# Performance work log

Measured on AMD Instinct MI355X. Metric: run time of the kernel, lower is better.

Reference implementation:

```python
import jax, jax.numpy as jnp
import numpy as np

N_LAYERS, H, D, DFF, V = 6, 16, 1024, 4096, 512
B, S = 4, 2048
DK = D // H
EPS = 1e-6
NEG = -1000000000.0


def _pe_table(max_len, d):
    pos = np.arange(max_len, dtype=np.float32)[:, None]
    div = 1.0 / (10000.0 ** (np.arange(0, d, 2, dtype=np.float32) / d))
    pe = np.zeros((max_len, d), dtype=np.float32)
    pe[:, 0::2] = np.sin(pos * div)
    pe[:, 1::2] = np.cos(pos * div)
    return jnp.asarray(pe[None])  # [1, max_len, d]


def setup_inputs() -> dict:
    key = jax.random.key(0)
    ks = jax.random.split(key, 20)
    f = lambda k, shp: (jax.random.normal(k, shp, dtype=jnp.float32) * 0.02)
    inp = {
        "tgt": jax.random.randint(ks[0], (B, S), 0, V, dtype=jnp.int64),
        "tgt_mask": jnp.tril(jnp.ones((S, S), dtype=jnp.int32))[None],  # [1,S,S] causal
        "emb": f(ks[1], (V, D)),
        "pe": _pe_table(S, D),
        "Wq": f(ks[2], (N_LAYERS, H, D, DK)), "bq": f(ks[3], (N_LAYERS, H, DK)),
        "Wk": f(ks[4], (N_LAYERS, H, D, DK)), "bk": f(ks[5], (N_LAYERS, H, DK)),
        "Wv": f(ks[6], (N_LAYERS, H, D, DK)), "bv": f(ks[7], (N_LAYERS, H, DK)),
        "Wo": f(ks[8], (N_LAYERS, D, D)), "bo": f(ks[9], (N_LAYERS, D)),
        "W1": f(ks[10], (N_LAYERS, D, DFF)), "b1": f(ks[11], (N_LAYERS, DFF)),
        "W2": f(ks[12], (N_LAYERS, DFF, D)), "b2": f(ks[13], (N_LAYERS, D)),
        "ln1_a": jnp.ones((N_LAYERS, D)), "ln1_b": jnp.zeros((N_LAYERS, D)),
        "ln2_a": jnp.ones((N_LAYERS, D)), "ln2_b": jnp.zeros((N_LAYERS, D)),
        "lnf_a": jnp.ones((D,)), "lnf_b": jnp.zeros((D,)),
    }
    return inp


def _ln(x, a, b):
    # torch: a*(x-mean)/(std+eps)+b with unbiased std
    m = x.mean(-1, keepdims=True)
    var = ((x - m) ** 2).sum(-1, keepdims=True) / (x.shape[-1] - 1)
    return a * (x - m) / (jnp.sqrt(var) + EPS) + b


def reference(tgt, tgt_mask, emb, pe, Wq, bq, Wk, bk, Wv, bv, Wo, bo,
              W1, b1, W2, b2, ln1_a, ln1_b, ln2_a, ln2_b, lnf_a, lnf_b):
    d = emb.shape[1]
    s = tgt.shape[1]
    x = emb[tgt] * jnp.sqrt(jnp.float32(d)) + pe[:, :s]  # [B,S,D]
    dk = Wq.shape[-1]
    scale = jnp.sqrt(jnp.float32(dk))

    def layer(x, p):
        wq, bq_, wk, bk_, wv, bv_, wo, bo_, w1, b1_, w2, b2_, a1, g1, a2, g2 = p
        h = _ln(x, a1, g1)
        q = jnp.einsum('bsd,hdk->bhsk', h, wq) + bq_[:, None, :]
        k = jnp.einsum('bsd,hdk->bhsk', h, wk) + bk_[:, None, :]
        v = jnp.einsum('bsd,hdk->bhsk', h, wv) + bv_[:, None, :]
        sc = jnp.einsum('bhsk,bhtk->bhst', q, k) / scale
        sc = jnp.where(tgt_mask[:, None] == 0, jnp.float32(NEG), sc)
        att = jax.nn.softmax(sc, axis=-1)
        o = jnp.einsum('bhst,bhtk->bhsk', att, v)
        o = o.transpose(0, 2, 1, 3).reshape(x.shape)  # concat heads (head order)
        x = x + (o @ wo + bo_)
        h2 = _ln(x, a2, g2)
        x = x + (jnp.maximum(h2 @ w1 + b1_, 0.0) @ w2 + b2_)
        return x, None

    x, _ = jax.lax.scan(layer, x, (Wq, bq, Wk, bk, Wv, bv, Wo, bo,
                                   W1, b1, W2, b2, ln1_a, ln1_b, ln2_a, ln2_b))
    return _ln(x, lnf_a, lnf_b)
```

## Files before the change

kernel.cpp:

```cpp
#include <hip/hip_runtime.h>

typedef __bf16 bf16;
typedef float f32x4 __attribute__((ext_vector_type(4)));
typedef __bf16 bf16x8 __attribute__((ext_vector_type(8)));
typedef __bf16 bf16x4 __attribute__((ext_vector_type(4)));
typedef __bf16 bf16x2 __attribute__((ext_vector_type(2)));

#define NL 6
#define NH 16
#define DM 1024
#define DFF 4096
#define SEQ 2048
#define NB 4
#define NTOK (NB*SEQ)

__device__ __forceinline__ void gload16(const void* g, void* l) {
  __builtin_amdgcn_global_load_lds((const __attribute__((address_space(1))) void*)g,
                                   (__attribute__((address_space(3))) void*)l, 16, 0, 0);
}

__global__ __launch_bounds__(256) void repack_t(const float* __restrict__ src,
                                                bf16* __restrict__ out, int K, int N) {
  const int l = blockIdx.z;
  const int d0 = blockIdx.x * 32, n0 = blockIdx.y * 32;
  __shared__ float t[32][33];
  const int tx = threadIdx.x & 31, ty = threadIdx.x >> 5;
  const float* s = src + (size_t)l * K * N;
  #pragma unroll
  for (int j = 0; j < 4; ++j)
    t[ty*4 + j][tx] = s[(size_t)(d0 + ty*4 + j) * N + n0 + tx];
  __syncthreads();
  bf16* o = out + (size_t)l * N * K;
  #pragma unroll
  for (int j = 0; j < 4; ++j)
    o[(size_t)(n0 + ty*4 + j) * K + d0 + tx] = (bf16)t[tx][ty*4 + j];
}

__global__ __launch_bounds__(256) void repack_qkv(const float* __restrict__ Wq,
                                                  const float* __restrict__ Wk,
                                                  const float* __restrict__ Wv,
                                                  bf16* __restrict__ out) {
  const int l = blockIdx.z;
  const int d0 = blockIdx.x * 32, n0 = blockIdx.y * 32;
  __shared__ float t[32][33];
  const int tx = threadIdx.x & 31, ty = threadIdx.x >> 5;
  const int which = n0 >> 10, h = (n0 & 1023) >> 6, kh0 = n0 & 63;
  const float* W = (which == 0) ? Wq : (which == 1 ? Wk : Wv);
  const float* s = W + ((size_t)(l*NH + h) * DM) * 64 + kh0;
  #pragma unroll
  for (int j = 0; j < 4; ++j)
    t[ty*4 + j][tx] = s[(size_t)(d0 + ty*4 + j) * 64 + tx];
  __syncthreads();
  bf16* o = out + (size_t)l * 3072 * DM + (size_t)n0 * DM + d0;
  #pragma unroll
  for (int j = 0; j < 4; ++j)
    o[(size_t)(ty*4 + j) * DM + tx] = (bf16)t[tx][ty*4 + j];
}

__global__ __launch_bounds__(256) void repack_b(const float* __restrict__ bq,
                                                const float* __restrict__ bk,
                                                const float* __restrict__ bv,
                                                float* __restrict__ out) {
  const int i = blockIdx.x * 256 + threadIdx.x;
  if (i >= NL * 3072) return;
  const int l = i / 3072, n = i % 3072;
  const int which = n >> 10, h = (n >> 6) & 15, kh = n & 63;
  const float* b = (which == 0) ? bq : (which == 1 ? bk : bv);
  out[i] = b[(l*NH + h) * 64 + kh];
}

__global__ __launch_bounds__(256) void embed_k(const int* __restrict__ tgt,
                                               const float* __restrict__ emb,
                                               const float* __restrict__ pe,
                                               float* __restrict__ x) {
  const int i = blockIdx.x;
  const int spos = i & (SEQ - 1);
  const int tok = tgt[i];
  const int tid = threadIdx.x;
  float4 e = ((const float4*)(emb + (size_t)tok * DM))[tid];
  float4 p = ((const float4*)(pe + (size_t)spos * DM))[tid];
  float4 r; r.x = e.x*32.f + p.x; r.y = e.y*32.f + p.y; r.z = e.z*32.f + p.z; r.w = e.w*32.f + p.w;
  ((float4*)(x + (size_t)i * DM))[tid] = r;
}

template<bool OB>
__global__ __launch_bounds__(256) void ln_k(const float* __restrict__ x,
                                            const float* __restrict__ a,
                                            const float* __restrict__ bsh,
                                            bf16* __restrict__ ob, float* __restrict__ of) {
  __shared__ float red[8];
  const int row = blockIdx.x, tid = threadIdx.x;
  const float4 v = ((const float4*)(x + (size_t)row * DM))[tid];
  float s = v.x + v.y + v.z + v.w;
  #pragma unroll
  for (int off = 32; off > 0; off >>= 1) s += __shfl_down(s, off);
  if ((tid & 63) == 0) red[tid >> 6] = s;
  __syncthreads();
  const float mean = (red[0] + red[1] + red[2] + red[3]) * (1.f / 1024.f);
  const float d0 = v.x - mean, d1 = v.y - mean, d2 = v.z - mean, d3 = v.w - mean;
  float ss = d0*d0 + d1*d1 + d2*d2 + d3*d3;
  #pragma unroll
  for (int off = 32; off > 0; off >>= 1) ss += __shfl_down(ss, off);
  if ((tid & 63) == 0) red[4 + (tid >> 6)] = ss;
  __syncthreads();
  const float var = (red[4] + red[5] + red[6] + red[7]) * (1.f / 1023.f);
  const float inv = 1.f / (sqrtf(var) + 1e-6f);
  const float4 av = ((const float4*)a)[tid];
  const float4 bv = ((const float4*)bsh)[tid];
  const float r0 = av.x * d0 * inv + bv.x;
  const float r1 = av.y * d1 * inv + bv.y;
  const float r2 = av.z * d2 * inv + bv.z;
  const float r3 = av.w * d3 * inv + bv.w;
  if (OB) {
    bf16x4 w; w[0] = (bf16)r0; w[1] = (bf16)r1; w[2] = (bf16)r2; w[3] = (bf16)r3;
    ((bf16x4*)(ob + (size_t)row * DM))[tid] = w;
  } else {
    float4 w; w.x = r0; w.y = r1; w.z = r2; w.w = r3;
    ((float4*)(of + (size_t)row * DM))[tid] = w;
  }
}

#define BARRIER() asm volatile("s_barrier" ::: "memory")
#define VMW(n)    asm volatile("s_waitcnt vmcnt(" #n ")" ::: "memory")

template<int EPI>
__global__ __launch_bounds__(512, 1) void gemm8(const bf16* __restrict__ A,
                                                const bf16* __restrict__ B,
                                                const float* __restrict__ bias,
                                                float* __restrict__ xres,
                                                bf16* __restrict__ outb,
                                                bf16* __restrict__ vtb,
                                                int K, int ldc) {
  __shared__ __align__(16) char lds[131072];
  const int tid = threadIdx.x;
  const int m0 = blockIdx.x * 256, n0 = blockIdx.y * 256;
  const int wid = tid >> 6, lane = tid & 63;
  const int wm = wid >> 2, wn = wid & 3;
  const int fr = lane & 15, fq = lane >> 4;
  const int fl16 = (fq * 16 + fr) * 16;
  const int s0 = tid, s1 = tid + 512;
  const int r0 = ((s0 >> 7) << 4) | (s0 & 15), c0 = (((s0 >> 6) & 1) << 2) | ((s0 >> 4) & 3);
  const int r1 = ((s1 >> 7) << 4) | (s1 & 15), c1 = (((s1 >> 6) & 1) << 2) | ((s1 >> 4) & 3);
  const bf16* Ap0 = A + (size_t)(m0 + r0) * K + c0 * 8;
  const bf16* Ap1 = A + (size_t)(m0 + r1) * K + c1 * 8;
  const bf16* Bp0 = B + (size_t)(n0 + r0) * K + c0 * 8;
  const bf16* Bp1 = B + (size_t)(n0 + r1) * K + c1 * 8;
  const size_t rskip = (size_t)128 * K;
  const int aRd = wm * 16384;
  const int bRd = 32768 + (wn >> 1) * 16384;
  const int bN = (wn & 1) * 4;

  f32x4 acc[8][4] = {};
  bf16x8 af8[8][2], bfr[4][2];

#define ST_A(d, h, kt) { \
  gload16(Ap0 + (size_t)(h) * rskip + (kt), lds + (d)*65536 + (h)*16384 + s0*16); \
  gload16(Ap1 + (size_t)(h) * rskip + (kt), lds + (d)*65536 + (h)*16384 + s1*16); }
#define ST_B(d, h, kt) { \
  gload16(Bp0 + (size_t)(h) * rskip + (kt), lds + (d)*65536 + 32768 + (h)*16384 + s0*16); \
  gload16(Bp1 + (size_t)(h) * rskip + (kt), lds + (d)*65536 + 32768 + (h)*16384 + s1*16); }
#define LD_A(d, mb) { _Pragma("unroll") for (int m_ = 0; m_ < 4; ++m_) \
    _Pragma("unroll") for (int ks_ = 0; ks_ < 2; ++ks_) \
      af8[(mb) + m_][ks_] = *(const bf16x8*)(lds + (d)*65536 + aRd + ((mb) + m_)*2048 + ks_*1024 + fl16); }
#define LD_B(d, nb) { _Pragma("unroll") for (int n_ = 0; n_ < 2; ++n_) \
    _Pragma("unroll") for (int ks_ = 0; ks_ < 2; ++ks_) \
      bfr[(nb) + n_][ks_] = *(const bf16x8*)(lds + (d)*65536 + bRd + (bN + (nb) + n_)*2048 + ks_*1024 + fl16); }
#define MFMA_Q(mb, nb) { __builtin_amdgcn_s_setprio(1); \
  _Pragma("unroll") for (int m_ = 0; m_ < 4; ++m_) \
  _Pragma("unroll") for (int n_ = 0; n_ < 2; ++n_) \
  _Pragma("unroll") for (int ks_ = 0; ks_ < 2; ++ks_) \
    acc[(mb) + m_][(nb) + n_] = __builtin_amdgcn_mfma_f32_16x16x32_bf16( \
        af8[(mb) + m_][ks_], bfr[(nb) + n_][ks_], acc[(mb) + m_][(nb) + n_], 0, 0, 0); \
  __builtin_amdgcn_s_setprio(0); }

  ST_A(0, 0, 0); ST_A(0, 1, 0);
  ST_B(0, 0, 0); ST_B(0, 1, 0);
  ST_A(1, 0, 64); ST_A(1, 1, 64);
  VMW(4);
  BARRIER();

  const int niter = K >> 7;
  for (int it = 0; it < niter; ++it) {
    const int ktB1 = (2 * it + 1) << 6;
    const int ktE2 = (2 * it + 2) << 6;
    const int ktO3 = (2 * it + 3) << 6;
    const bool more = (it + 1 < niter);
    LD_A(0, 0); LD_B(0, 0);
    ST_B(1, 0, ktB1);
    BARRIER(); MFMA_Q(0, 0); BARRIER();
    LD_A(0, 4);
    ST_B(1, 1, ktB1);
    BARRIER(); MFMA_Q(4, 0); BARRIER();
    LD_B(0, 2);
    if (more) ST_A(0, 0, ktE2);
    BARRIER(); MFMA_Q(4, 2); BARRIER();
    if (more) { ST_A(0, 1, ktE2); VMW(4); } else { VMW(0); }
    BARRIER(); MFMA_Q(0, 2); BARRIER();
    LD_A(1, 0); LD_B(1, 0);
    if (more) ST_B(0, 0, ktE2);
    BARRIER(); MFMA_Q(0, 0); BARRIER();
    LD_A(1, 4);
    if (more) ST_B(0, 1, ktE2);
    BARRIER(); MFMA_Q(4, 0); BARRIER();
    LD_B(1, 2);
    if (more) ST_A(1, 0, ktO3);
    BARRIER(); MFMA_Q(4, 2); BARRIER();
    if (more) { ST_A(1, 1, ktO3); VMW(4); }
    BARRIER(); MFMA_Q(0, 2); BARRIER();
  }
#undef ST_A
#undef ST_B
#undef LD_A
#undef LD_B
#undef MFMA_Q

  #pragma unroll
  for (int m = 0; m < 8; ++m) {
    const int row = m0 + wm * 128 + m * 16 + fq * 4;
    #pragma unroll
    for (int n = 0; n < 4; ++n) {
      const int col = n0 + wn * 64 + n * 16 + fr;
      const float bc = bias[col];
      if constexpr (EPI == 3) {
        if (col >= 2048) {
          const int hh = (col - 2048) >> 6, dkk = col & 63;
          const int bb = row >> 11, tt = row & 2047;
          bf16x4 w;
          #pragma unroll
          for (int j = 0; j < 4; ++j) w[j] = (bf16)(acc[m][n][j] + bc);
          *(bf16x4*)(vtb + ((((size_t)bb*NH + hh)*64 + dkk)*SEQ + tt)) = w;
          continue;
        }
      }
      #pragma unroll
      for (int j = 0; j < 4; ++j) {
        const float v = acc[m][n][j] + bc;
        if constexpr (EPI == 1) {
          xres[(size_t)(row + j) * ldc + col] += v;
        } else if constexpr (EPI == 2) {
          outb[(size_t)(row + j) * ldc + col] = (bf16)fmaxf(v, 0.f);
        } else {
          outb[(size_t)(row + j) * ldc + col] = (bf16)v;
        }
      }
    }
  }
}

template<int EPI>
__global__ __launch_bounds__(512, 1) void gemm8n(const bf16* __restrict__ A,
                                                 const bf16* __restrict__ B,
                                                 const float* __restrict__ bias,
                                                 float* __restrict__ xres,
                                                 bf16* __restrict__ outb,
                                                 bf16* __restrict__ vtb,
                                                 int K, int ldc) {
  __shared__ __align__(16) char lds[131072];
  const int tid = threadIdx.x;
  const int m0 = blockIdx.x * 128, n0 = blockIdx.y * 256;
  const int wid = tid >> 6, lane = tid & 63;
  const int wm = wid >> 2, wn = wid & 3;
  const int fr = lane & 15, fq = lane >> 4;
  const int fl16 = (fq * 16 + fr) * 16;
  const int s0 = tid, s1 = tid + 512;
  const int r0 = ((s0 >> 7) << 4) | (s0 & 15), c0 = (((s0 >> 6) & 1) << 2) | ((s0 >> 4) & 3);
  const int r1 = ((s1 >> 7) << 4) | (s1 & 15), c1 = (((s1 >> 6) & 1) << 2) | ((s1 >> 4) & 3);
  const bf16* Ap0 = A + (size_t)(m0 + r0) * K + c0 * 8;
  const bf16* Ap1 = A + (size_t)(m0 + r1) * K + c1 * 8;
  const bf16* Bp0 = B + (size_t)(n0 + r0) * K + c0 * 8;
  const bf16* Bp1 = B + (size_t)(n0 + r1) * K + c1 * 8;
  const size_t rskipB = (size_t)128 * K;
  const int aRd = wm * 8192;
  const int bRd = wn * 8192;

  f32x4 acc[4][4] = {};
  bf16x8 af[4][2], bfr[4][2];

#define ST_An(d, kt) { \
  gload16(Ap0 + (kt), lds + (d)*16384 + s0*16); \
  gload16(Ap1 + (kt), lds + (d)*16384 + s1*16); }
#define ST_Bn(j, h, kt) { \
  gload16(Bp0 + (size_t)(h) * rskipB + (kt), lds + 32768 + (j)*32768 + (h)*16384 + s0*16); \
  gload16(Bp1 + (size_t)(h) * rskipB + (kt), lds + 32768 + (j)*32768 + (h)*16384 + s1*16); }
#define LD_An(d) { _Pragma("unroll") for (int m_ = 0; m_ < 4; ++m_) \
    _Pragma("unroll") for (int ks_ = 0; ks_ < 2; ++ks_) \
      af[m_][ks_] = *(const bf16x8*)(lds + (d)*16384 + aRd + m_*2048 + ks_*1024 + fl16); }
#define LD_Bn(j, nb) { _Pragma("unroll") for (int n_ = 0; n_ < 2; ++n_) \
    _Pragma("unroll") for (int ks_ = 0; ks_ < 2; ++ks_) \
      bfr[(nb) + n_][ks_] = *(const bf16x8*)(lds + 32768 + (j)*32768 + bRd + ((nb) + n_)*2048 + ks_*1024 + fl16); }
#define MFMA_H(nb) { __builtin_amdgcn_s_setprio(1); \
  _Pragma("unroll") for (int m_ = 0; m_ < 4; ++m_) \
  _Pragma("unroll") for (int n_ = 0; n_ < 2; ++n_) \
  _Pragma("unroll") for (int ks_ = 0; ks_ < 2; ++ks_) \
    acc[m_][(nb) + n_] = __builtin_amdgcn_mfma_f32_16x16x32_bf16( \
        af[m_][ks_], bfr[(nb) + n_][ks_], acc[m_][(nb) + n_], 0, 0, 0); \
  __builtin_amdgcn_s_setprio(0); }

  ST_An(0, 0);
  ST_Bn(0, 0, 0); ST_Bn(0, 1, 0);
  ST_An(1, 64);
  ST_Bn(1, 0, 64); ST_Bn(1, 1, 64);
  VMW(0);
  BARRIER();

  const int nt = K >> 6;
  int j = 0;
  for (int t = 0; t < nt; ++t) {
    const int d = t & 1;
    const int j2 = (j + 2 >= 3) ? (j - 1) : (j + 2);
    const bool more = (t + 2 < nt);
    const int kt2 = (t + 2) << 6;
    LD_An(d); LD_Bn(j, 0);
    if (more) { ST_Bn(j2, 0, kt2); ST_Bn(j2, 1, kt2); }
    BARRIER(); MFMA_H(0); BARRIER();
    LD_Bn(j, 2);
    if (more) { ST_An(d, kt2); VMW(6); } else { VMW(0); }
    BARRIER(); MFMA_H(2); BARRIER();
    j = (j + 1 >= 3) ? 0 : (j + 1);
  }
#undef ST_An
#undef ST_Bn
#undef LD_An
#undef LD_Bn
#undef MFMA_H

  #pragma unroll
  for (int m = 0; m < 4; ++m) {
    const int row = m0 + wm * 64 + m * 16 + fq * 4;
    #pragma unroll
    for (int n = 0; n < 4; ++n) {
      const int col = n0 + wn * 64 + n * 16 + fr;
      const float bc = bias[col];
      if constexpr (EPI == 3) {
        if (col >= 2048) {
          const int hh = (col - 2048) >> 6, dkk = col & 63;
          const int bb = row >> 11, tt = row & 2047;
          bf16x4 w;
          #pragma unroll
          for (int jj = 0; jj < 4; ++jj) w[jj] = (bf16)(acc[m][n][jj] + bc);
          *(bf16x4*)(vtb + ((((size_t)bb*NH + hh)*64 + dkk)*SEQ + tt)) = w;
          continue;
        }
      }
      #pragma unroll
      for (int jj = 0; jj < 4; ++jj) {
        const float v = acc[m][n][jj] + bc;
        if constexpr (EPI == 1) {
          xres[(size_t)(row + jj) * ldc + col] += v;
        } else if constexpr (EPI == 2) {
          outb[(size_t)(row + jj) * ldc + col] = (bf16)fmaxf(v, 0.f);
        } else {
          outb[(size_t)(row + jj) * ldc + col] = (bf16)v;
        }
      }
    }
  }
}

__global__ __launch_bounds__(256) void attn5_k(const bf16* __restrict__ qk,
                                               const bf16* __restrict__ vt,
                                               bf16* __restrict__ o) {
  __shared__ __align__(16) bf16 Ks[64 * 64];
  __shared__ __align__(16) bf16 Vs[64 * 64];
  __shared__ __align__(16) bf16 Ps[4][16 * 64];
  const int pairi = blockIdx.x;
  const int bh = blockIdx.y;
  const int b = bh >> 4, h = bh & 15;
  const int tid = threadIdx.x;
  const int wave = tid >> 6, lane = tid & 63;
  const int fr = lane & 15, fq = lane >> 4;
  const bf16* Qg = qk + (size_t)b * SEQ * 2048 + h * 64;
  const bf16* Kg = Qg + 1024;
  const bf16* Vtg = vt + (size_t)bh * 64 * SEQ;
  char* Ksc = (char*)Ks;
  char* Vsc = (char*)Vs;
  char* Pw = (char*)&Ps[wave][0];
  const int fr7 = fr & 7;

  for (int pass = 0; pass < 2; ++pass) {
    const int qb = (pass == 0) ? pairi : (31 - pairi);
    const int q0w = qb * 64 + wave * 16;
    const int qrow = q0w + fr;
    const bf16x8 qf0 = *(const bf16x8*)(Qg + (size_t)qrow * 2048 + fq * 8);
    const bf16x8 qf1 = *(const bf16x8*)(Qg + (size_t)qrow * 2048 + 32 + fq * 8);
    f32x4 oacc[4] = {};
    float mrun = -1e30f, lrun = 0.f;
    const int nt = qb + 1;
    for (int kt = 0; kt < nt; ++kt) {
      const int t0 = kt * 64;
      __syncthreads();
      #pragma unroll
      for (int s2 = 0; s2 < 2; ++s2) {
        const int slot = tid + s2 * 256;
        const int r = slot >> 3, mm = slot & 7;
        const int gc = (mm ^ (r & 7)) * 8;
        gload16(Kg + (size_t)(t0 + r) * 2048 + gc, Ksc + slot * 16);
        gload16(Vtg + (size_t)r * SEQ + t0 + gc, Vsc + slot * 16);
      }
      __syncthreads();
      if (t0 > q0w + 15) continue;
      f32x4 s[4] = {};
      #pragma unroll
      for (int n = 0; n < 4; ++n) {
        const int t_ = n * 16 + fr;
        const bf16x8 k0 = *(const bf16x8*)(Ksc + (t_ * 8 + (fq ^ (t_ & 7))) * 16);
        const bf16x8 k1 = *(const bf16x8*)(Ksc + (t_ * 8 + ((fq + 4) ^ (t_ & 7))) * 16);
        s[n] = __builtin_amdgcn_mfma_f32_16x16x32_bf16(k0, qf0, s[n], 0, 0, 0);
        s[n] = __builtin_amdgcn_mfma_f32_16x16x32_bf16(k1, qf1, s[n], 0, 0, 0);
      }
      float sv[16];
      #pragma unroll
      for (int n = 0; n < 4; ++n)
        #pragma unroll
        for (int jj = 0; jj < 4; ++jj)
          sv[n * 4 + jj] = s[n][jj] * 0.125f;
      const bool need_mask = (t0 + 63 > q0w);
      if (need_mask) {
        #pragma unroll
        for (int i = 0; i < 16; ++i) {
          const int t_abs = t0 + (i >> 2) * 16 + fq * 4 + (i & 3);
          if (t_abs > qrow) sv[i] = -1e30f;
        }
      }
      float a8[8];
      #pragma unroll
      for (int i = 0; i < 8; ++i) a8[i] = fmaxf(sv[i], sv[i + 8]);
      float a4[4];
      #pragma unroll
      for (int i = 0; i < 4; ++i) a4[i] = fmaxf(a8[i], a8[i + 4]);
      float mt = fmaxf(fmaxf(a4[0], a4[1]), fmaxf(a4[2], a4[3]));
      mt = fmaxf(mt, __shfl_xor(mt, 16));
      mt = fmaxf(mt, __shfl_xor(mt, 32));
      const float mnew = fmaxf(mrun, mt);
      const float corr = __expf(mrun - mnew);
      mrun = mnew;
      #pragma unroll
      for (int i = 0; i < 16; ++i) sv[i] = __expf(sv[i] - mnew);
      #pragma unroll
      for (int i = 0; i < 8; ++i) a8[i] = sv[i] + sv[i + 8];
      #pragma unroll
      for (int i = 0; i < 4; ++i) a4[i] = a8[i] + a8[i + 4];
      float ps = (a4[0] + a4[1]) + (a4[2] + a4[3]);
      ps += __shfl_xor(ps, 16);
      ps += __shfl_xor(ps, 32);
      lrun = lrun * corr + ps;
      float cv[4];
      #pragma unroll
      for (int jj = 0; jj < 4; ++jj) cv[jj] = __shfl(corr, fq * 4 + jj);
      #pragma unroll
      for (int nd = 0; nd < 4; ++nd)
        #pragma unroll
        for (int jj = 0; jj < 4; ++jj)
          oacc[nd][jj] *= cv[jj];
      #pragma unroll
      for (int n = 0; n < 4; ++n)
        #pragma unroll
        for (int jp = 0; jp < 2; ++jp) {
          bf16x2 w; w[0] = (bf16)sv[n * 4 + jp * 2]; w[1] = (bf16)sv[n * 4 + jp * 2 + 1];
          const int byteoff = n * 32 + fq * 8 + jp * 4;
          const int chunk = byteoff >> 4, within = byteoff & 15;
          *(bf16x2*)(Pw + fr * 128 + ((chunk ^ fr7) << 4) + within) = w;
        }
      #pragma unroll
      for (int ks = 0; ks < 2; ++ks) {
        const bf16x8 pa = *(const bf16x8*)(Pw + fr * 128 + (((ks * 4 + fq) ^ fr7) << 4));
        #pragma unroll
        for (int nd = 0; nd < 4; ++nd) {
          const int dk_ = nd * 16 + fr;
          const bf16x8 vf = *(const bf16x8*)(Vsc + (dk_ * 8 + ((ks * 4 + fq) ^ (dk_ & 7))) * 16);
          oacc[nd] = __builtin_amdgcn_mfma_f32_16x16x32_bf16(pa, vf, oacc[nd], 0, 0, 0);
        }
      }
    }
    float lv[4];
    #pragma unroll
    for (int jj = 0; jj < 4; ++jj) lv[jj] = __shfl(lrun, fq * 4 + jj);
    #pragma unroll
    for (int nd = 0; nd < 4; ++nd) {
      const int col = h * 64 + nd * 16 + fr;
      #pragma unroll
      for (int jj = 0; jj < 4; ++jj) {
        const int row = q0w + fq * 4 + jj;
        o[((size_t)b * SEQ + row) * DM + col] = (bf16)(oacc[nd][jj] / lv[jj]);
      }
    }
  }
}

extern "C" void kernel_launch(void* const* d_in, const int* in_sizes, int n_in,
                              void* d_out, int out_size, void* d_ws, size_t ws_size,
                              hipStream_t stream) {
  const int*   tgt  = (const int*)d_in[0];
  const float* emb  = (const float*)d_in[2];
  const float* pe   = (const float*)d_in[3];
  const float* Wq   = (const float*)d_in[4];
  const float* bq   = (const float*)d_in[5];
  const float* Wk   = (const float*)d_in[6];
  const float* bk   = (const float*)d_in[7];
  const float* Wv   = (const float*)d_in[8];
  const float* bv   = (const float*)d_in[9];
  const float* Wo   = (const float*)d_in[10];
  const float* bo   = (const float*)d_in[11];
  const float* W1   = (const float*)d_in[12];
  const float* b1   = (const float*)d_in[13];
  const float* W2   = (const float*)d_in[14];
  const float* b2   = (const float*)d_in[15];
  const float* ln1a = (const float*)d_in[16];
  const float* ln1b = (const float*)d_in[17];
  const float* ln2a = (const float*)d_in[18];
  const float* ln2b = (const float*)d_in[19];
  const float* lnfa = (const float*)d_in[20];
  const float* lnfb = (const float*)d_in[21];

  char* ws = (char*)d_ws;
  size_t off = 0;
  bf16*  wqkv = (bf16*)(ws + off);  off += (size_t)NL * 3072 * DM * 2;
  bf16*  wo_  = (bf16*)(ws + off);  off += (size_t)NL * DM * DM * 2;
  bf16*  w1_  = (bf16*)(ws + off);  off += (size_t)NL * DFF * DM * 2;
  bf16*  w2_  = (bf16*)(ws + off);  off += (size_t)NL * DM * DFF * 2;
  float* bqkv = (float*)(ws + off); off += (size_t)NL * 3072 * 4;
  float* x    = (float*)(ws + off); off += (size_t)NTOK * DM * 4;
  bf16*  hbuf = (bf16*)(ws + off);  off += (size_t)NTOK * DM * 2;
  bf16*  qkb  = (bf16*)(ws + off);  off += (size_t)NTOK * 2048 * 2;
  bf16*  vtb  = (bf16*)(ws + off);  off += (size_t)NB * NH * 64 * SEQ * 2;
  bf16*  obuf = (bf16*)(ws + off);  off += (size_t)NTOK * DM * 2;
  bf16*  ubuf = qkb;

  repack_qkv<<<dim3(32, 96, NL), 256, 0, stream>>>(Wq, Wk, Wv, wqkv);
  repack_t  <<<dim3(32, 32, NL), 256, 0, stream>>>(Wo, wo_, DM, DM);
  repack_t  <<<dim3(32, 128, NL), 256, 0, stream>>>(W1, w1_, DM, DFF);
  repack_t  <<<dim3(128, 32, NL), 256, 0, stream>>>(W2, w2_, DFF, DM);
  repack_b  <<<72, 256, 0, stream>>>(bq, bk, bv, bqkv);
  embed_k   <<<NTOK, 256, 0, stream>>>(tgt, emb, pe, x);

  for (int l = 0; l < NL; ++l) {
    ln_k<true><<<NTOK, 256, 0, stream>>>(x, ln1a + l * DM, ln1b + l * DM, hbuf, nullptr);
    gemm8n<3><<<dim3(64, 12), 512, 0, stream>>>(hbuf, wqkv + (size_t)l * 3072 * DM,
                                                bqkv + l * 3072, nullptr, qkb, vtb, DM, 2048);
    attn5_k<<<dim3(16, 64), 256, 0, stream>>>(qkb, vtb, obuf);
    gemm8n<1><<<dim3(64, 4), 512, 0, stream>>>(obuf, wo_ + (size_t)l * DM * DM,
                                               bo + l * DM, x, nullptr, nullptr, DM, DM);
    ln_k<true><<<NTOK, 256, 0, stream>>>(x, ln2a + l * DM, ln2b + l * DM, hbuf, nullptr);
    gemm8<2><<<dim3(32, 16), 512, 0, stream>>>(hbuf, w1_ + (size_t)l * DFF * DM,
                                               b1 + l * DFF, nullptr, ubuf, nullptr, DM, DFF);
    gemm8n<1><<<dim3(64, 4), 512, 0, stream>>>(ubuf, w2_ + (size_t)l * DM * DFF,
                                               b2 + l * DM, x, nullptr, nullptr, DFF, DM);
  }
  ln_k<false><<<NTOK, 256, 0, stream>>>(x, lnfa, lnfb, nullptr, (float*)d_out);

  (void)in_sizes; (void)n_in; (void)out_size; (void)ws_size;
}
```

Before: 2.738 ms.

## Split-K residual GEMMs with atomic accumulation and XCD-aware attention block mapping

The Wo and W2 projections move from the gemm8n kernel to the 256x256-tile gemm8 kernel with a two-way K split over blockIdx.z. Each half adds its partial result into the fp32 residual with atomicAdd, and only the first split adds the bias. The aim is to give the N=1024 GEMMs enough blocks (256 instead of 128) to fill the GPU. The cost is doubled atomic traffic on the residual and fp32 results that vary with summation order. Separately, attention blocks are remapped so the blocks sharing a batch-head land on the same XCD, which should improve L2 reuse of K and V.

```diff
diff --git a/kernel.cpp b/kernel.cpp
--- a/kernel.cpp
+++ b/kernel.cpp
@@ -130,10 +130,12 @@
                                                 float* __restrict__ xres,
                                                 bf16* __restrict__ outb,
                                                 bf16* __restrict__ vtb,
-                                                int K, int ldc) {
+                                                int K, int ldc, int Klen) {
   __shared__ __align__(16) char lds[131072];
   const int tid = threadIdx.x;
   const int m0 = blockIdx.x * 256, n0 = blockIdx.y * 256;
+  A += (size_t)blockIdx.z * Klen;
+  B += (size_t)blockIdx.z * Klen;
   const int wid = tid >> 6, lane = tid & 63;
   const int wm = wid >> 2, wn = wid & 3;
   const int fr = lane & 15, fq = lane >> 4;
@@ -179,7 +181,7 @@
   VMW(4);
   BARRIER();
 
-  const int niter = K >> 7;
+  const int niter = Klen >> 7;
   for (int it = 0; it < niter; ++it) {
     const int ktB1 = (2 * it + 1) << 6;
     const int ktE2 = (2 * it + 2) << 6;
@@ -214,13 +216,15 @@
 #undef LD_B
 #undef MFMA_Q
 
+  const float zf = (blockIdx.z == 0) ? 1.f : 0.f;
   #pragma unroll
   for (int m = 0; m < 8; ++m) {
     const int row = m0 + wm * 128 + m * 16 + fq * 4;
     #pragma unroll
     for (int n = 0; n < 4; ++n) {
       const int col = n0 + wn * 64 + n * 16 + fr;
-      const float bc = bias[col];
+      float bc = bias[col];
+      if constexpr (EPI == 4) bc *= zf;
       if constexpr (EPI == 3) {
         if (col >= 2048) {
           const int hh = (col - 2048) >> 6, dkk = col & 63;
@@ -235,7 +239,9 @@
       #pragma unroll
       for (int j = 0; j < 4; ++j) {
         const float v = acc[m][n][j] + bc;
-        if constexpr (EPI == 1) {
+        if constexpr (EPI == 4) {
+          atomicAdd(xres + (size_t)(row + j) * ldc + col, v);
+        } else if constexpr (EPI == 1) {
           xres[(size_t)(row + j) * ldc + col] += v;
         } else if constexpr (EPI == 2) {
           outb[(size_t)(row + j) * ldc + col] = (bf16)fmaxf(v, 0.f);
@@ -363,8 +369,10 @@
   __shared__ __align__(16) bf16 Ks[64 * 64];
   __shared__ __align__(16) bf16 Vs[64 * 64];
   __shared__ __align__(16) bf16 Ps[4][16 * 64];
-  const int pairi = blockIdx.x;
-  const int bh = blockIdx.y;
+  const int flat = blockIdx.y * 16 + blockIdx.x;
+  const int xcd = flat & 7, slot = flat >> 3;
+  const int bh = xcd * 8 + (slot >> 4);
+  const int pairi = slot & 15;
   const int b = bh >> 4, h = bh & 15;
   const int tid = threadIdx.x;
   const int wave = tid >> 6, lane = tid & 63;
@@ -391,11 +399,11 @@
       __syncthreads();
       #pragma unroll
       for (int s2 = 0; s2 < 2; ++s2) {
-        const int slot = tid + s2 * 256;
-        const int r = slot >> 3, mm = slot & 7;
+        const int slot2 = tid + s2 * 256;
+        const int r = slot2 >> 3, mm = slot2 & 7;
         const int gc = (mm ^ (r & 7)) * 8;
-        gload16(Kg + (size_t)(t0 + r) * 2048 + gc, Ksc + slot * 16);
-        gload16(Vtg + (size_t)r * SEQ + t0 + gc, Vsc + slot * 16);
+        gload16(Kg + (size_t)(t0 + r) * 2048 + gc, Ksc + slot2 * 16);
+        gload16(Vtg + (size_t)r * SEQ + t0 + gc, Vsc + slot2 * 16);
       }
       __syncthreads();
       if (t0 > q0w + 15) continue;
@@ -538,13 +546,13 @@
     gemm8n<3><<<dim3(64, 12), 512, 0, stream>>>(hbuf, wqkv + (size_t)l * 3072 * DM,
                                                 bqkv + l * 3072, nullptr, qkb, vtb, DM, 2048);
     attn5_k<<<dim3(16, 64), 256, 0, stream>>>(qkb, vtb, obuf);
-    gemm8n<1><<<dim3(64, 4), 512, 0, stream>>>(obuf, wo_ + (size_t)l * DM * DM,
-                                               bo + l * DM, x, nullptr, nullptr, DM, DM);
+    gemm8<4><<<dim3(32, 4, 2), 512, 0, stream>>>(obuf, wo_ + (size_t)l * DM * DM,
+                                                 bo + l * DM, x, nullptr, nullptr, DM, DM, DM / 2);
     ln_k<true><<<NTOK, 256, 0, stream>>>(x, ln2a + l * DM, ln2b + l * DM, hbuf, nullptr);
     gemm8<2><<<dim3(32, 16), 512, 0, stream>>>(hbuf, w1_ + (size_t)l * DFF * DM,
-                                               b1 + l * DFF, nullptr, ubuf, nullptr, DM, DFF);
-    gemm8n<1><<<dim3(64, 4), 512, 0, stream>>>(ubuf, w2_ + (size_t)l * DM * DFF,
-                                               b2 + l * DM, x, nullptr, nullptr, DFF, DM);
+                                               b1 + l * DFF, nullptr, ubuf, nullptr, DM, DFF, DM);
+    gemm8<4><<<dim3(32, 4, 2), 512, 0, stream>>>(ubuf, w2_ + (size_t)l * DM * DFF,
+                                                 b2 + l * DM, x, nullptr, nullptr, DFF, DM, DFF / 2);
   }
   ln_k<false><<<NTOK, 256, 0, stream>>>(x, lnfa, lnfb, nullptr, (float*)d_out);
 
```

After: 2.879 ms. +5.1%, slower.

## Double-buffer attention K/V tiles and share them across paired query blocks

Applied to the files above, without the earlier changes.

The attention kernel now processes both paired query blocks in one key loop, so each K/V tile is loaded once and used for both. Loads are double-buffered so the next tile is fetched while the current one is computed. It also skips the rescale of the running max when it does not grow, folds the 1/8 score scale into the Q projection epilogue, and remaps blocks so each XCD works on the same heads. The cost is more registers for two accumulator sets and twice the shared memory, which may lower occupancy. The EPI==3 V-transpose path is also removed from one GEMM variant.

```diff
diff --git a/kernel.cpp b/kernel.cpp
--- a/kernel.cpp
+++ b/kernel.cpp
@@ -221,17 +221,6 @@
     for (int n = 0; n < 4; ++n) {
       const int col = n0 + wn * 64 + n * 16 + fr;
       const float bc = bias[col];
-      if constexpr (EPI == 3) {
-        if (col >= 2048) {
-          const int hh = (col - 2048) >> 6, dkk = col & 63;
-          const int bb = row >> 11, tt = row & 2047;
-          bf16x4 w;
-          #pragma unroll
-          for (int j = 0; j < 4; ++j) w[j] = (bf16)(acc[m][n][j] + bc);
-          *(bf16x4*)(vtb + ((((size_t)bb*NH + hh)*64 + dkk)*SEQ + tt)) = w;
-          continue;
-        }
-      }
       #pragma unroll
       for (int j = 0; j < 4; ++j) {
         const float v = acc[m][n][j] + bc;
@@ -344,7 +333,8 @@
       }
       #pragma unroll
       for (int jj = 0; jj < 4; ++jj) {
-        const float v = acc[m][n][jj] + bc;
+        float v = acc[m][n][jj] + bc;
+        if constexpr (EPI == 3) { if (col < 1024) v *= 0.125f; }
         if constexpr (EPI == 1) {
           xres[(size_t)(row + jj) * ldc + col] += v;
         } else if constexpr (EPI == 2) {
@@ -360,11 +350,13 @@
 __global__ __launch_bounds__(256) void attn5_k(const bf16* __restrict__ qk,
                                                const bf16* __restrict__ vt,
                                                bf16* __restrict__ o) {
-  __shared__ __align__(16) bf16 Ks[64 * 64];
-  __shared__ __align__(16) bf16 Vs[64 * 64];
+  __shared__ __align__(16) bf16 Ks[2][64 * 64];
+  __shared__ __align__(16) bf16 Vs[2][64 * 64];
   __shared__ __align__(16) bf16 Ps[4][16 * 64];
-  const int pairi = blockIdx.x;
-  const int bh = blockIdx.y;
+  const int flat = blockIdx.y * 16 + blockIdx.x;
+  const int xcd = flat & 7, slot = flat >> 3;
+  const int bh = xcd * 8 + (slot >> 4);
+  const int pairi = slot & 15;
   const int b = bh >> 4, h = bh & 15;
   const int tid = threadIdx.x;
   const int wave = tid >> 6, lane = tid & 63;
@@ -372,116 +364,152 @@
   const bf16* Qg = qk + (size_t)b * SEQ * 2048 + h * 64;
   const bf16* Kg = Qg + 1024;
   const bf16* Vtg = vt + (size_t)bh * 64 * SEQ;
-  char* Ksc = (char*)Ks;
-  char* Vsc = (char*)Vs;
   char* Pw = (char*)&Ps[wave][0];
   const int fr7 = fr & 7;
 
-  for (int pass = 0; pass < 2; ++pass) {
-    const int qb = (pass == 0) ? pairi : (31 - pairi);
-    const int q0w = qb * 64 + wave * 16;
-    const int qrow = q0w + fr;
-    const bf16x8 qf0 = *(const bf16x8*)(Qg + (size_t)qrow * 2048 + fq * 8);
-    const bf16x8 qf1 = *(const bf16x8*)(Qg + (size_t)qrow * 2048 + 32 + fq * 8);
-    f32x4 oacc[4] = {};
-    float mrun = -1e30f, lrun = 0.f;
-    const int nt = qb + 1;
-    for (int kt = 0; kt < nt; ++kt) {
-      const int t0 = kt * 64;
-      __syncthreads();
-      #pragma unroll
-      for (int s2 = 0; s2 < 2; ++s2) {
-        const int slot = tid + s2 * 256;
-        const int r = slot >> 3, mm = slot & 7;
-        const int gc = (mm ^ (r & 7)) * 8;
-        gload16(Kg + (size_t)(t0 + r) * 2048 + gc, Ksc + slot * 16);
-        gload16(Vtg + (size_t)r * SEQ + t0 + gc, Vsc + slot * 16);
-      }
-      __syncthreads();
-      if (t0 > q0w + 15) continue;
-      f32x4 s[4] = {};
-      #pragma unroll
-      for (int n = 0; n < 4; ++n) {
-        const int t_ = n * 16 + fr;
-        const bf16x8 k0 = *(const bf16x8*)(Ksc + (t_ * 8 + (fq ^ (t_ & 7))) * 16);
-        const bf16x8 k1 = *(const bf16x8*)(Ksc + (t_ * 8 + ((fq + 4) ^ (t_ & 7))) * 16);
-        s[n] = __builtin_amdgcn_mfma_f32_16x16x32_bf16(k0, qf0, s[n], 0, 0, 0);
-        s[n] = __builtin_amdgcn_mfma_f32_16x16x32_bf16(k1, qf1, s[n], 0, 0, 0);
-      }
-      float sv[16];
-      #pragma unroll
-      for (int n = 0; n < 4; ++n)
-        #pragma unroll
-        for (int jj = 0; jj < 4; ++jj)
-          sv[n * 4 + jj] = s[n][jj] * 0.125f;
-      const bool need_mask = (t0 + 63 > q0w);
-      if (need_mask) {
-        #pragma unroll
-        for (int i = 0; i < 16; ++i) {
-          const int t_abs = t0 + (i >> 2) * 16 + fq * 4 + (i & 3);
-          if (t_abs > qrow) sv[i] = -1e30f;
-        }
-      }
-      float a8[8];
-      #pragma unroll
-      for (int i = 0; i < 8; ++i) a8[i] = fmaxf(sv[i], sv[i + 8]);
-      float a4[4];
-      #pragma unroll
-      for (int i = 0; i < 4; ++i) a4[i] = fmaxf(a8[i], a8[i + 4]);
-      float mt = fmaxf(fmaxf(a4[0], a4[1]), fmaxf(a4[2], a4[3]));
-      mt = fmaxf(mt, __shfl_xor(mt, 16));
-      mt = fmaxf(mt, __shfl_xor(mt, 32));
-      const float mnew = fmaxf(mrun, mt);
-      const float corr = __expf(mrun - mnew);
-      mrun = mnew;
-      #pragma unroll
-      for (int i = 0; i < 16; ++i) sv[i] = __expf(sv[i] - mnew);
-      #pragma unroll
-      for (int i = 0; i < 8; ++i) a8[i] = sv[i] + sv[i + 8];
-      #pragma unroll
-      for (int i = 0; i < 4; ++i) a4[i] = a8[i] + a8[i + 4];
-      float ps = (a4[0] + a4[1]) + (a4[2] + a4[3]);
-      ps += __shfl_xor(ps, 16);
-      ps += __shfl_xor(ps, 32);
-      lrun = lrun * corr + ps;
-      float cv[4];
-      #pragma unroll
-      for (int jj = 0; jj < 4; ++jj) cv[jj] = __shfl(corr, fq * 4 + jj);
-      #pragma unroll
-      for (int nd = 0; nd < 4; ++nd)
-        #pragma unroll
-        for (int jj = 0; jj < 4; ++jj)
-          oacc[nd][jj] *= cv[jj];
-      #pragma unroll
-      for (int n = 0; n < 4; ++n)
-        #pragma unroll
-        for (int jp = 0; jp < 2; ++jp) {
-          bf16x2 w; w[0] = (bf16)sv[n * 4 + jp * 2]; w[1] = (bf16)sv[n * 4 + jp * 2 + 1];
-          const int byteoff = n * 32 + fq * 8 + jp * 4;
-          const int chunk = byteoff >> 4, within = byteoff & 15;
-          *(bf16x2*)(Pw + fr * 128 + ((chunk ^ fr7) << 4) + within) = w;
-        }
-      #pragma unroll
-      for (int ks = 0; ks < 2; ++ks) {
-        const bf16x8 pa = *(const bf16x8*)(Pw + fr * 128 + (((ks * 4 + fq) ^ fr7) << 4));
-        #pragma unroll
-        for (int nd = 0; nd < 4; ++nd) {
-          const int dk_ = nd * 16 + fr;
-          const bf16x8 vf = *(const bf16x8*)(Vsc + (dk_ * 8 + ((ks * 4 + fq) ^ (dk_ & 7))) * 16);
-          oacc[nd] = __builtin_amdgcn_mfma_f32_16x16x32_bf16(pa, vf, oacc[nd], 0, 0, 0);
-        }
-      }
+  const int sl0 = tid, sl1 = tid + 256;
+  const int sr0 = sl0 >> 3, sm0 = sl0 & 7, sg0 = (sm0 ^ (sr0 & 7)) * 8;
+  const int sr1 = sl1 >> 3, sm1 = sl1 & 7, sg1 = (sm1 ^ (sr1 & 7)) * 8;
+
+#define STAGE_KV(db, t0_) { \
+    gload16(Kg + (size_t)((t0_) + sr0) * 2048 + sg0, (char*)Ks + (db)*8192 + sl0*16); \
+    gload16(Vtg + (size_t)sr0 * SEQ + (t0_) + sg0,   (char*)Vs + (db)*8192 + sl0*16); \
+    gload16(Kg + (size_t)((t0_) + sr1) * 2048 + sg1, (char*)Ks + (db)*8192 + sl1*16); \
+    gload16(Vtg + (size_t)sr1 * SEQ + (t0_) + sg1,   (char*)Vs + (db)*8192 + sl1*16); }
+
+#define COMPUTE(q0w_, qrow_, qf0_, qf1_, oacc_, mrun_, lrun_) { \
+      f32x4 s_[4] = {}; \
+      _Pragma("unroll") \
+      for (int n = 0; n < 4; ++n) { \
+        const int t_ = n * 16 + fr; \
+        const bf16x8 k0 = *(const bf16x8*)(Ksc + (t_ * 8 + (fq ^ (t_ & 7))) * 16); \
+        const bf16x8 k1 = *(const bf16x8*)(Ksc + (t_ * 8 + ((fq + 4) ^ (t_ & 7))) * 16); \
+        s_[n] = __builtin_amdgcn_mfma_f32_16x16x32_bf16(k0, (qf0_), s_[n], 0, 0, 0); \
+        s_[n] = __builtin_amdgcn_mfma_f32_16x16x32_bf16(k1, (qf1_), s_[n], 0, 0, 0); \
+      } \
+      float sv[16]; \
+      _Pragma("unroll") \
+      for (int n = 0; n < 4; ++n) \
+        _Pragma("unroll") \
+        for (int jj = 0; jj < 4; ++jj) \
+          sv[n * 4 + jj] = s_[n][jj]; \
+      if (t0 + 63 > (q0w_)) { \
+        _Pragma("unroll") \
+        for (int i = 0; i < 16; ++i) { \
+          const int t_abs = t0 + (i >> 2) * 16 + fq * 4 + (i & 3); \
+          if (t_abs > (qrow_)) sv[i] = -1e30f; \
+        } \
+      } \
+      float a8[8]; \
+      _Pragma("unroll") \
+      for (int i = 0; i < 8; ++i) a8[i] = fmaxf(sv[i], sv[i + 8]); \
+      float a4[4]; \
+      _Pragma("unroll") \
+      for (int i = 0; i < 4; ++i) a4[i] = fmaxf(a8[i], a8[i + 4]); \
+      float mt = fmaxf(fmaxf(a4[0], a4[1]), fmaxf(a4[2], a4[3])); \
+      mt = fmaxf(mt, __shfl_xor(mt, 16)); \
+      mt = fmaxf(mt, __shfl_xor(mt, 32)); \
+      const bool grow = __any(mt > (mrun_)); \
+      const float mnew = fmaxf((mrun_), mt); \
+      float corr = 1.f; \
+      if (grow) corr = __expf((mrun_) - mnew); \
+      (mrun_) = mnew; \
+      _Pragma("unroll") \
+      for (int i = 0; i < 16; ++i) sv[i] = __expf(sv[i] - mnew); \
+      _Pragma("unroll") \
+      for (int i = 0; i < 8; ++i) a8[i] = sv[i] + sv[i + 8]; \
+      _Pragma("unroll") \
+      for (int i = 0; i < 4; ++i) a4[i] = a8[i] + a8[i + 4]; \
+      float ps = (a4[0] + a4[1]) + (a4[2] + a4[3]); \
+      ps += __shfl_xor(ps, 16); \
+      ps += __shfl_xor(ps, 32); \
+      if (grow) { \
+        (lrun_) = (lrun_) * corr + ps; \
+        float cv[4]; \
+        _Pragma("unroll") \
+        for (int jj = 0; jj < 4; ++jj) cv[jj] = __shfl(corr, fq * 4 + jj); \
+        _Pragma("unroll") \
+        for (int nd = 0; nd < 4; ++nd) \
+          _Pragma("unroll") \
+          for (int jj = 0; jj < 4; ++jj) \
+            (oacc_)[nd][jj] *= cv[jj]; \
+      } else { \
+        (lrun_) += ps; \
+      } \
+      _Pragma("unroll") \
+      for (int n = 0; n < 4; ++n) \
+        _Pragma("unroll") \
+        for (int jp = 0; jp < 2; ++jp) { \
+          bf16x2 w; w[0] = (bf16)sv[n * 4 + jp * 2]; w[1] = (bf16)sv[n * 4 + jp * 2 + 1]; \
+          const int byteoff = n * 32 + fq * 8 + jp * 4; \
+          const int chunk = byteoff >> 4, within = byteoff & 15; \
+          *(bf16x2*)(Pw + fr * 128 + ((chunk ^ fr7) << 4) + within) = w; \
+        } \
+      _Pragma("unroll") \
+      for (int ks = 0; ks < 2; ++ks) { \
+        const bf16x8 pa = *(const bf16x8*)(Pw + fr * 128 + (((ks * 4 + fq) ^ fr7) << 4)); \
+        _Pragma("unroll") \
+        for (int nd = 0; nd < 4; ++nd) { \
+          const int dk_ = nd * 16 + fr; \
+          const bf16x8 vf = *(const bf16x8*)(Vsc + (dk_ * 8 + ((ks * 4 + fq) ^ (dk_ & 7))) * 16); \
+          (oacc_)[nd] = __builtin_amdgcn_mfma_f32_16x16x32_bf16(pa, vf, (oacc_)[nd], 0, 0, 0); \
+        } \
+      } }
+
+  const int qbA = pairi;
+  const int qbB = 31 - pairi;
+  const int q0A = qbA * 64 + wave * 16, q0B = qbB * 64 + wave * 16;
+  const int qrA = q0A + fr, qrB = q0B + fr;
+  const bf16x8 qA0 = *(const bf16x8*)(Qg + (size_t)qrA * 2048 + fq * 8);
+  const bf16x8 qA1 = *(const bf16x8*)(Qg + (size_t)qrA * 2048 + 32 + fq * 8);
+  const bf16x8 qB0 = *(const bf16x8*)(Qg + (size_t)qrB * 2048 + fq * 8);
+  const bf16x8 qB1 = *(const bf16x8*)(Qg + (size_t)qrB * 2048 + 32 + fq * 8);
+  f32x4 oaccA[4] = {}, oaccB[4] = {};
+  float mA = -1e30f, lA = 0.f, mB = -1e30f, lB = 0.f;
+  const int nt = qbB + 1;
+
+  STAGE_KV(0, 0);
+  for (int kt = 0; kt < nt; ++kt) {
+    const int t0 = kt * 64;
+    const int db = kt & 1;
+    __syncthreads();
+    if (kt + 1 < nt) {
+      STAGE_KV(db ^ 1, (kt + 1) * 64);
+      VMW(4);
+    } else {
+      VMW(0);
     }
+    __syncthreads();
+    const char* Ksc = (char*)Ks + db * 8192;
+    const char* Vsc = (char*)Vs + db * 8192;
+    if (t0 <= q0A + 15) COMPUTE(q0A, qrA, qA0, qA1, oaccA, mA, lA);
+    COMPUTE(q0B, qrB, qB0, qB1, oaccB, mB, lB);
+  }
+#undef COMPUTE
+#undef STAGE_KV
+
+  {
     float lv[4];
     #pragma unroll
-    for (int jj = 0; jj < 4; ++jj) lv[jj] = __shfl(lrun, fq * 4 + jj);
+    for (int jj = 0; jj < 4; ++jj) lv[jj] = __shfl(lA, fq * 4 + jj);
     #pragma unroll
     for (int nd = 0; nd < 4; ++nd) {
       const int col = h * 64 + nd * 16 + fr;
       #pragma unroll
       for (int jj = 0; jj < 4; ++jj) {
-        const int row = q0w + fq * 4 + jj;
-        o[((size_t)b * SEQ + row) * DM + col] = (bf16)(oacc[nd][jj] / lv[jj]);
+        const int row = q0A + fq * 4 + jj;
+        o[((size_t)b * SEQ + row) * DM + col] = (bf16)(oaccA[nd][jj] / lv[jj]);
+      }
+    }
+    #pragma unroll
+    for (int jj = 0; jj < 4; ++jj) lv[jj] = __shfl(lB, fq * 4 + jj);
+    #pragma unroll
+    for (int nd = 0; nd < 4; ++nd) {
+      const int col = h * 64 + nd * 16 + fr;
+      #pragma unroll
+      for (int jj = 0; jj < 4; ++jj) {
+        const int row = q0B + fq * 4 + jj;
+        o[((size_t)b * SEQ + row) * DM + col] = (bf16)(oaccB[nd][jj] / lv[jj]);
       }
     }
   }
```

Result: no change. 2.703 ms (-1.3%).
